# Kernel tuning notes

Measured on AMD Instinct MI355X. Metric: run time of the kernel, lower is better.

## Reference

```python
import jax, jax.numpy as jnp
import numpy as np

N = 50000      # nodes
E = 800000     # edges (avg degree 16)
IN = 128       # in_feats
HID = 32       # hidden_feats per head
H = 4          # num_heads
NEG_SLOPE = 0.2


def setup_inputs() -> dict:
    key = jax.random.key(0)
    ks = jax.random.split(key, 13)
    x = jax.random.normal(ks[0], (N, IN), jnp.float32)
    src = jax.random.randint(ks[1], (E,), 0, N, jnp.int32)
    dst = jax.random.randint(ks[2], (E,), 0, N, jnp.int32)

    def lin(k, fi, fo):
        return jax.random.normal(k, (fi, fo), jnp.float32) * (1.0 / np.sqrt(fi))

    # conv1: IN -> H*HID
    W1 = lin(ks[3], IN, H * HID)
    al1 = jax.random.normal(ks[4], (H, HID), jnp.float32) * 0.1
    ar1 = jax.random.normal(ks[5], (H, HID), jnp.float32) * 0.1
    b1 = jnp.zeros((H, HID), jnp.float32)
    # conv2: H*HID -> H*HID
    W2 = lin(ks[6], H * HID, H * HID)
    al2 = jax.random.normal(ks[7], (H, HID), jnp.float32) * 0.1
    ar2 = jax.random.normal(ks[8], (H, HID), jnp.float32) * 0.1
    b2 = jnp.zeros((H, HID), jnp.float32)
    # fc: HID -> 1
    fcW = lin(ks[9], HID, 1)
    fcb = jnp.zeros((1,), jnp.float32)
    return {"x": x, "src": src, "dst": dst,
            "W1": W1, "al1": al1, "ar1": ar1, "b1": b1,
            "W2": W2, "al2": al2, "ar2": ar2, "b2": b2,
            "fcW": fcW, "fcb": fcb}


def gat_conv(x, src, dst, W, al, ar, b):
    # x: [N, F_in] -> feat: [N, H, HID]
    feat = (x @ W).reshape(N, H, HID)
    el = jnp.sum(feat * al, axis=-1)            # [N, H]
    er = jnp.sum(feat * ar, axis=-1)            # [N, H]
    e = jax.nn.leaky_relu(el[src] + er[dst], NEG_SLOPE)  # [E, H]
    # segment softmax over incoming edges of each dst node
    m = jax.ops.segment_max(e, dst, num_segments=N)      # [N, H]
    ex = jnp.exp(e - m[dst])                              # [E, H]
    denom = jax.ops.segment_sum(ex, dst, num_segments=N)  # [N, H]
    alpha = ex / denom[dst]                                # [E, H]
    msg = feat[src] * alpha[:, :, None]                    # [E, H, HID]
    out = jax.ops.segment_sum(msg, dst, num_segments=N)   # [N, H, HID]
    return out + b[None, :, :]


def reference(x, src, dst, W1, al1, ar1, b1, W2, al2, ar2, b2, fcW, fcb):
    h = gat_conv(x, src, dst, W1, al1, ar1, b1).reshape(N, H * HID)
    h = jax.nn.relu(h)
    # dropout(0.5) is identity in eval mode
    h = gat_conv(h, src, dst, W2, al2, ar2, b2).mean(axis=1)  # [N, HID]
    return h @ fcW + fcb                                       # [N, 1]
```

## Files before the change

### kernel.cpp

```cpp
#include <hip/hip_runtime.h>
#include <hip/hip_fp16.h>

#define LEAK 0.2f
#define CAP 64
#define CS 16

static __device__ inline int swz(int c, int j) {
    int qb = j >> 3, r = j & 7;
    return c * 144 + qb * 8 + (qb >> 2) * 4 + r;
}
static __device__ inline unsigned q4(float4 v, float is) {
    int x0 = __float2int_rn(v.x * is) + 128; x0 = min(max(x0, 0), 255);
    int x1 = __float2int_rn(v.y * is) + 128; x1 = min(max(x1, 0), 255);
    int x2 = __float2int_rn(v.z * is) + 128; x2 = min(max(x2, 0), 255);
    int x3 = __float2int_rn(v.w * is) + 128; x3 = min(max(x3, 0), 255);
    return (unsigned)x0 | ((unsigned)x1 << 8) | ((unsigned)x2 << 16) | ((unsigned)x3 << 24);
}

__global__ __launch_bounds__(256) void k0(
    int* __restrict__ cnt,
    const float* __restrict__ W2, const float* __restrict__ al2,
    const float* __restrict__ ar2, const float* __restrict__ fcW,
    const float* __restrict__ b2, float* __restrict__ WfT,
    float* __restrict__ bc, int N, int zb) {
    const int b = blockIdx.x;
    const int t = threadIdx.x;
    if (b < zb) {
        int i = b * 256 + t;
        if (i < N * (CS / 4)) ((int4*)cnt)[i] = make_int4(0, 0, 0, 0);
        return;
    }
    int idx = (b - zb) * 256 + t;
    if (idx < 1536) {
        int c = idx >> 7, k = idx & 127;
        int h = c & 3, sel = c >> 2;
        const float* vec = (sel == 0) ? (al2 + 32 * h)
                         : (sel == 1) ? (ar2 + 32 * h) : fcW;
        float s = 0.f;
#pragma unroll 8
        for (int m = 0; m < 32; m++) s += W2[k * 128 + 32 * h + m] * vec[m];
        WfT[c * 128 + k] = s;
    } else if (idx < 1540) {
        int h = idx - 1536;
        float s = 0.f;
        for (int m = 0; m < 32; m++) s += b2[h * 32 + m] * fcW[m];
        bc[h] = s;
    }
}

__global__ __launch_bounds__(256) void k_ell(
    const int* __restrict__ src, const int* __restrict__ dst,
    int* __restrict__ cnt, unsigned short* __restrict__ ell,
    int E, int N, int R) {
    const int part = blockIdx.x & 7;
    const int rank = blockIdx.x >> 3;
    const int S = (N + 7) >> 3;
    const int lo = part * S;
    const int hi = (lo + S < N) ? (lo + S) : N;
    const int per = (E + R - 1) / R;
    const int e0 = rank * per;
    const int e1 = (e0 + per < E) ? (e0 + per) : E;
    int e = e0 + threadIdx.x;
    for (; e + 768 < e1; e += 1024) {
        int d0 = dst[e];       int d1 = dst[e + 256];
        int d2 = dst[e + 512]; int d3 = dst[e + 768];
        if (d0 >= lo && d0 < hi) {
            int pos = atomicAdd(&cnt[d0 * CS], 1);
            if (pos < CAP) ell[(size_t)d0 * CAP + pos] = (unsigned short)src[e];
        }
        if (d1 >= lo && d1 < hi) {
            int pos = atomicAdd(&cnt[d1 * CS], 1);
            if (pos < CAP) ell[(size_t)d1 * CAP + pos] = (unsigned short)src[e + 256];
        }
        if (d2 >= lo && d2 < hi) {
            int pos = atomicAdd(&cnt[d2 * CS], 1);
            if (pos < CAP) ell[(size_t)d2 * CAP + pos] = (unsigned short)src[e + 512];
        }
        if (d3 >= lo && d3 < hi) {
            int pos = atomicAdd(&cnt[d3 * CS], 1);
            if (pos < CAP) ell[(size_t)d3 * CAP + pos] = (unsigned short)src[e + 768];
        }
    }
    for (; e < e1; e += 256) {
        int d = dst[e];
        if (d >= lo && d < hi) {
            int pos = atomicAdd(&cnt[d * CS], 1);
            if (pos < CAP) ell[(size_t)d * CAP + pos] = (unsigned short)src[e];
        }
    }
}

__global__ __launch_bounds__(256, 4) void k1g(
    const float* __restrict__ X, const float* __restrict__ W,
    const float* __restrict__ al, const float* __restrict__ ar,
    float2* __restrict__ elsc2, float* __restrict__ er_nh,
    unsigned* __restrict__ fq8, int N) {
    __shared__ float sW[32 * 128];
    __shared__ float sXT[32 * 64];
    const int t = threadIdx.x;
    const int r0 = blockIdx.x * 64;
    const int tx = t & 15;
    const int ty = t >> 4;
    const float4* X4 = (const float4*)X;
    const float4* W4 = (const float4*)W;
    float4* sW4 = (float4*)sW;
    const float4* sXT4 = (const float4*)sXT;

    float4 acc[4][2];
#pragma unroll
    for (int r = 0; r < 4; r++) {
        acc[r][0] = make_float4(0.f, 0.f, 0.f, 0.f);
        acc[r][1] = make_float4(0.f, 0.f, 0.f, 0.f);
    }
    for (int ks = 0; ks < 4; ++ks) {
        if (ks) __syncthreads();
#pragma unroll
        for (int i = 0; i < 4; i++) {
            int idx = i * 256 + t;
            sW4[idx] = W4[1024 * ks + idx];
        }
#pragma unroll
        for (int i = 0; i < 2; i++) {
            int idx = i * 256 + t;
            int row = idx >> 3;
            int kq = idx & 7;
            float4 v = make_float4(0.f, 0.f, 0.f, 0.f);
            if (r0 + row < N) v = X4[(size_t)(r0 + row) * 32 + ks * 8 + kq];
            int sc = ((row >> 2) ^ kq) * 4 + (row & 3);
            sXT[(4 * kq + 0) * 64 + sc] = v.x;
            sXT[(4 * kq + 1) * 64 + sc] = v.y;
            sXT[(4 * kq + 2) * 64 + sc] = v.z;
            sXT[(4 * kq + 3) * 64 + sc] = v.w;
        }
        __syncthreads();
#pragma unroll 4
        for (int k = 0; k < 32; k++) {
            float4 w0 = sW4[k * 32 + tx];
            float4 w1 = sW4[k * 32 + 16 + tx];
            float4 x0 = sXT4[k * 16 + (ty ^ (k >> 2))];
            float xs[4] = {x0.x, x0.y, x0.z, x0.w};
#pragma unroll
            for (int r = 0; r < 4; r++) {
                acc[r][0].x += xs[r] * w0.x; acc[r][0].y += xs[r] * w0.y;
                acc[r][0].z += xs[r] * w0.z; acc[r][0].w += xs[r] * w0.w;
                acc[r][1].x += xs[r] * w1.x; acc[r][1].y += xs[r] * w1.y;
                acc[r][1].z += xs[r] * w1.z; acc[r][1].w += xs[r] * w1.w;
            }
        }
    }
    const float4* al4p = (const float4*)al;
    const float4* ar4p = (const float4*)ar;
    float4 alA = al4p[tx], alB = al4p[16 + tx];
    float4 arA = ar4p[tx], arB = ar4p[16 + tx];
#pragma unroll
    for (int r = 0; r < 4; r++) {
        int row = r0 + ty * 4 + r;
        bool ok = row < N;
        float4 a0 = acc[r][0], a1 = acc[r][1];
        float m = fmaxf(fmaxf(fmaxf(fabsf(a0.x), fabsf(a0.y)),
                              fmaxf(fabsf(a0.z), fabsf(a0.w))),
                        fmaxf(fmaxf(fabsf(a1.x), fabsf(a1.y)),
                              fmaxf(fabsf(a1.z), fabsf(a1.w))));
#pragma unroll
        for (int off = 1; off < 16; off <<= 1) m = fmaxf(m, __shfl_xor(m, off));
        float scale = m * (1.f / 127.f);
        float is = (m > 0.f) ? (127.f / m) : 0.f;
        if (ok) {
            fq8[(size_t)row * 32 + tx] = q4(a0, is);
            fq8[(size_t)row * 32 + 16 + tx] = q4(a1, is);
        }
        float elA = a0.x * alA.x + a0.y * alA.y + a0.z * alA.z + a0.w * alA.w;
        float erA = a0.x * arA.x + a0.y * arA.y + a0.z * arA.z + a0.w * arA.w;
        float elB = a1.x * alB.x + a1.y * alB.y + a1.z * alB.z + a1.w * alB.w;
        float erB = a1.x * arB.x + a1.y * arB.y + a1.z * arB.z + a1.w * arB.w;
#pragma unroll
        for (int off = 1; off < 8; off <<= 1) {
            elA += __shfl_xor(elA, off); erA += __shfl_xor(erA, off);
            elB += __shfl_xor(elB, off); erB += __shfl_xor(erB, off);
        }
        if (ok && tx == 0) {
            elsc2[row * 4 + 0] = make_float2(elA, scale);
            elsc2[row * 4 + 2] = make_float2(elB, scale);
            er_nh[row * 4 + 0] = erA;
            er_nh[row * 4 + 2] = erB;
        }
        if (ok && tx == 8) {
            elsc2[row * 4 + 1] = make_float2(elA, scale);
            elsc2[row * 4 + 3] = make_float2(elB, scale);
            er_nh[row * 4 + 1] = erA;
            er_nh[row * 4 + 3] = erB;
        }
    }
}

__global__ __launch_bounds__(256) void k_agg1P(
    const unsigned* __restrict__ fq8, const float2* __restrict__ elsc2,
    const float* __restrict__ er_nh, const unsigned short* __restrict__ ell,
    const int* __restrict__ cnt, const float* __restrict__ b1,
    const float* __restrict__ WfT, float2* __restrict__ Pag,
    float* __restrict__ er2, int N) {
    __shared__ float sWf[12 * 144];
    for (int i = threadIdx.x; i < 1536; i += 256)
        sWf[swz(i >> 7, i & 127)] = WfT[i];
    __syncthreads();
    const int wave = threadIdx.x >> 6, lane = threadIdx.x & 63;
    const int nsub = lane >> 4, q = lane & 15, h = q >> 2;
    const int wbase = q * 8 + (q >> 2) * 4;
    const uint2* fq2 = (const uint2*)fq8;

    const int n = blockIdx.x * 16 + wave * 4 + nsub;
    const bool nok = n < N;
    const int nc = nok ? n : (N - 1);
    int deg = nok ? cnt[n * CS] : 0; if (deg > CAP) deg = CAP;
    float er = nok ? er_nh[n * 4 + h] : 0.f;
    const unsigned short* row = ell + (size_t)nc * CAP;

    int dm = deg;
    dm = max(dm, __shfl_xor(dm, 16));
    dm = max(dm, __shfl_xor(dm, 32));

    float acc[8] = {0.f, 0.f, 0.f, 0.f, 0.f, 0.f, 0.f, 0.f};
    float den = 0.f, wss = 0.f;
    for (int jt = 0; jt < dm; jt += 16) {
        int s_all = (jt + q < CAP) ? (int)row[jt + q] : 0;
        int lim = dm - jt; if (lim > 16) lim = 16;
        for (int u = 0; u < lim; u += 8) {
            int sv[8]; float2 esv[8]; uint2 fv[8];
#pragma unroll
            for (int v = 0; v < 8; v++) {
                int jj = jt + u + v;
                int s = __shfl(s_all, (lane & 48) | ((u + v) & 15));
                sv[v] = (jj < deg) ? s : 0;
            }
#pragma unroll
            for (int v = 0; v < 8; v++) esv[v] = elsc2[sv[v] * 4 + h];
#pragma unroll
            for (int v = 0; v < 8; v++) fv[v] = fq2[(size_t)sv[v] * 16 + q];
#pragma unroll
            for (int v = 0; v < 8; v++) {
                int jj = jt + u + v;
                bool valid = jj < deg;
                float e = esv[v].x + er;
                e = fmaxf(e, LEAK * e);
                float w = valid ? __expf(e) : 0.f;
                float ws = w * esv[v].y;
                unsigned ua = fv[v].x, ub = fv[v].y;
                acc[0] += ws * (float)(ua & 0xff);
                acc[1] += ws * (float)((ua >> 8) & 0xff);
                acc[2] += ws * (float)((ua >> 16) & 0xff);
                acc[3] += ws * (float)(ua >> 24);
                acc[4] += ws * (float)(ub & 0xff);
                acc[5] += ws * (float)((ub >> 8) & 0xff);
                acc[6] += ws * (float)((ub >> 16) & 0xff);
                acc[7] += ws * (float)(ub >> 24);
                den += w; wss += ws;
            }
        }
    }
    float inv = (den > 0.f) ? (1.f / den) : 0.f;
    float off128 = 128.f * wss;
    float4 b1a = ((const float4*)b1)[q * 2];
    float4 b1b = ((const float4*)b1)[q * 2 + 1];
    float hv[8];
    hv[0] = fmaxf((acc[0] - off128) * inv + b1a.x, 0.f);
    hv[1] = fmaxf((acc[1] - off128) * inv + b1a.y, 0.f);
    hv[2] = fmaxf((acc[2] - off128) * inv + b1a.z, 0.f);
    hv[3] = fmaxf((acc[3] - off128) * inv + b1a.w, 0.f);
    hv[4] = fmaxf((acc[4] - off128) * inv + b1b.x, 0.f);
    hv[5] = fmaxf((acc[5] - off128) * inv + b1b.y, 0.f);
    hv[6] = fmaxf((acc[6] - off128) * inv + b1b.z, 0.f);
    hv[7] = fmaxf((acc[7] - off128) * inv + b1b.w, 0.f);
    float p[12];
#pragma unroll
    for (int c = 0; c < 12; c++) {
        const float* wr = sWf + c * 144 + wbase;
        float4 wa = *(const float4*)wr;
        float4 wb = *(const float4*)(wr + 4);
        p[c] = hv[0] * wa.x + hv[1] * wa.y + hv[2] * wa.z + hv[3] * wa.w
             + hv[4] * wb.x + hv[5] * wb.y + hv[6] * wb.z + hv[7] * wb.w;
    }
#pragma unroll
    for (int off = 1; off < 16; off <<= 1) {
#pragma unroll
        for (int c = 0; c < 12; c++) p[c] += __shfl_xor(p[c], off);
    }
    if (nok) {
        if (q < 4) Pag[(size_t)n * 4 + q] = make_float2(p[q], p[8 + q]);
        else if (q < 8) er2[(size_t)n * 4 + (q - 4)] = p[q];
    }
}

__global__ __launch_bounds__(256) void k_agg2(
    const float2* __restrict__ Pag, const float* __restrict__ er2,
    const unsigned short* __restrict__ ell, const int* __restrict__ cnt,
    const float* __restrict__ bc, const float* __restrict__ fcb,
    float* __restrict__ out, int N) {
    int idx = blockIdx.x * 256 + threadIdx.x;
    int n = idx >> 2, h = idx & 3;
    if (n >= N) return;
    int deg = cnt[n * CS]; if (deg > CAP) deg = CAP;
    float er = er2[(size_t)n * 4 + h];
    const unsigned short* row = ell + (size_t)n * CAP;
    float num = 0.f, den = 0.f;
    int j = 0, d8 = deg & ~7;
    for (; j < d8; j += 8) {
        ushort4 sa = *(const ushort4*)(row + j);
        ushort4 sb = *(const ushort4*)(row + j + 4);
        int sv[8] = {sa.x, sa.y, sa.z, sa.w, sb.x, sb.y, sb.z, sb.w};
        float2 g[8];
#pragma unroll
        for (int v = 0; v < 8; v++) g[v] = Pag[(size_t)sv[v] * 4 + h];
#pragma unroll
        for (int v = 0; v < 8; v++) {
            float e = g[v].x + er; e = fmaxf(e, LEAK * e);
            float w = __expf(e);
            num += w * g[v].y; den += w;
        }
    }
    for (; j < deg; ++j) {
        int s = row[j];
        float2 gg = Pag[(size_t)s * 4 + h];
        float e = gg.x + er; e = fmaxf(e, LEAK * e);
        float w = __expf(e);
        num += w * gg.y; den += w;
    }
    float r = (den > 0.f) ? (num / den) : 0.f;
    r += bc[h];
    r += __shfl_xor(r, 1);
    r += __shfl_xor(r, 2);
    if (h == 0) out[n] = 0.25f * r + fcb[0];
}

extern "C" void kernel_launch(void* const* d_in, const int* in_sizes, int n_in,
                              void* d_out, int out_size, void* d_ws, size_t ws_size,
                              hipStream_t stream) {
    const float* x   = (const float*)d_in[0];
    const int* src   = (const int*)d_in[1];
    const int* dst   = (const int*)d_in[2];
    const float* W1  = (const float*)d_in[3];
    const float* al1 = (const float*)d_in[4];
    const float* ar1 = (const float*)d_in[5];
    const float* b1  = (const float*)d_in[6];
    const float* W2  = (const float*)d_in[7];
    const float* al2 = (const float*)d_in[8];
    const float* ar2 = (const float*)d_in[9];
    const float* b2  = (const float*)d_in[10];
    const float* fcW = (const float*)d_in[11];
    const float* fcb = (const float*)d_in[12];
    float* out = (float*)d_out;

    const int N = in_sizes[0] / 128;
    const int E = in_sizes[1];

    char* w = (char*)d_ws;
    size_t off = 0;
    auto alloc = [&](size_t bytes) {
        void* p = w + off;
        off = (off + bytes + 255) & ~(size_t)255;
        return p;
    };
    unsigned* fq8  = (unsigned*)alloc((size_t)N * 32 * 4);
    float2* elsc2  = (float2*)alloc((size_t)N * 4 * 8);
    float* er_nh   = (float*)alloc((size_t)N * 4 * 4);
    float2* Pag    = (float2*)alloc((size_t)N * 4 * 8);
    float* er2     = (float*)alloc((size_t)N * 4 * 4);
    float* WfT     = (float*)alloc((size_t)(12 * 128 + 4) * 4);
    float* bc      = WfT + 12 * 128;
    int* cnt       = (int*)alloc((size_t)N * CS * 4);
    unsigned short* ell = (unsigned short*)alloc((size_t)N * CAP * 2);

    const int zb = (N * (CS / 4) + 255) / 256;
    const int gtiles = (N + 63) / 64;
    const int R = 256;

    k0<<<zb + 7, 256, 0, stream>>>(
        cnt, W2, al2, ar2, fcW, b2, WfT, bc, N, zb);
    k_ell<<<8 * R, 256, 0, stream>>>(src, dst, cnt, ell, E, N, R);
    k1g<<<gtiles, 256, 0, stream>>>(
        x, W1, al1, ar1, elsc2, er_nh, fq8, N);
    k_agg1P<<<(N + 15) / 16, 256, 0, stream>>>(
        fq8, elsc2, er_nh, ell, cnt, b1, WfT, Pag, er2, N);
    k_agg2<<<(N * 4 + 255) / 256, 256, 0, stream>>>(
        Pag, er2, ell, cnt, bc, fcb, out, N);
}
```

Baseline: 200.0 us.

## Fuse ELL build and first-layer GEMM into one interleaved launch

```diff
diff --git a/kernel.cpp b/kernel.cpp
--- a/kernel.cpp
+++ b/kernel.cpp
@@ -48,57 +48,65 @@
     }
 }
 
-__global__ __launch_bounds__(256) void k_ell(
-    const int* __restrict__ src, const int* __restrict__ dst,
-    int* __restrict__ cnt, unsigned short* __restrict__ ell,
-    int E, int N, int R) {
-    const int part = blockIdx.x & 7;
-    const int rank = blockIdx.x >> 3;
-    const int S = (N + 7) >> 3;
-    const int lo = part * S;
-    const int hi = (lo + S < N) ? (lo + S) : N;
-    const int per = (E + R - 1) / R;
-    const int e0 = rank * per;
-    const int e1 = (e0 + per < E) ? (e0 + per) : E;
-    int e = e0 + threadIdx.x;
-    for (; e + 768 < e1; e += 1024) {
-        int d0 = dst[e];       int d1 = dst[e + 256];
-        int d2 = dst[e + 512]; int d3 = dst[e + 768];
-        if (d0 >= lo && d0 < hi) {
-            int pos = atomicAdd(&cnt[d0 * CS], 1);
-            if (pos < CAP) ell[(size_t)d0 * CAP + pos] = (unsigned short)src[e];
-        }
-        if (d1 >= lo && d1 < hi) {
-            int pos = atomicAdd(&cnt[d1 * CS], 1);
-            if (pos < CAP) ell[(size_t)d1 * CAP + pos] = (unsigned short)src[e + 256];
-        }
-        if (d2 >= lo && d2 < hi) {
-            int pos = atomicAdd(&cnt[d2 * CS], 1);
-            if (pos < CAP) ell[(size_t)d2 * CAP + pos] = (unsigned short)src[e + 512];
-        }
-        if (d3 >= lo && d3 < hi) {
-            int pos = atomicAdd(&cnt[d3 * CS], 1);
-            if (pos < CAP) ell[(size_t)d3 * CAP + pos] = (unsigned short)src[e + 768];
-        }
-    }
-    for (; e < e1; e += 256) {
-        int d = dst[e];
-        if (d >= lo && d < hi) {
-            int pos = atomicAdd(&cnt[d * CS], 1);
-            if (pos < CAP) ell[(size_t)d * CAP + pos] = (unsigned short)src[e];
-        }
-    }
-}
-
-__global__ __launch_bounds__(256, 4) void k1g(
+__global__ __launch_bounds__(256, 4) void k_eg(
     const float* __restrict__ X, const float* __restrict__ W,
     const float* __restrict__ al, const float* __restrict__ ar,
     float2* __restrict__ elsc2, float* __restrict__ er_nh,
-    unsigned* __restrict__ fq8, int N) {
+    unsigned* __restrict__ fq8,
+    const int* __restrict__ src, const int* __restrict__ dst,
+    int* __restrict__ cnt, unsigned short* __restrict__ ell,
+    int N, int E, int R, int GO, int T) {
     __shared__ float sW[32 * 128];
     __shared__ float sXT[32 * 64];
+    const int b = blockIdx.x;
     const int t = threadIdx.x;
-    const int r0 = blockIdx.x * 64;
+    const int o = b >> 3;
+    const int g0 = (o * GO) / T;
+    const bool isGemm = ((o + 1) * GO) / T > g0;
+
+    if (!isGemm) {
+        const int part = b & 7;
+        const int rank = o - g0;
+        const int S = (N + 7) >> 3;
+        const int lo = part * S;
+        const int hi = (lo + S < N) ? (lo + S) : N;
+        const int per = (E + R - 1) / R;
+        const int e0 = rank * per;
+        const int e1 = (e0 + per < E) ? (e0 + per) : E;
+        int e = e0 + t;
+        for (; e + 768 < e1; e += 1024) {
+            int d0 = dst[e];       int d1 = dst[e + 256];
+            int d2 = dst[e + 512]; int d3 = dst[e + 768];
+            if (d0 >= lo && d0 < hi) {
+                int pos = atomicAdd(&cnt[d0 * CS], 1);
+                if (pos < CAP) ell[(size_t)d0 * CAP + pos] = (unsigned short)src[e];
+            }
+            if (d1 >= lo && d1 < hi) {
+                int pos = atomicAdd(&cnt[d1 * CS], 1);
+                if (pos < CAP) ell[(size_t)d1 * CAP + pos] = (unsigned short)src[e + 256];
+            }
+            if (d2 >= lo && d2 < hi) {
+                int pos = atomicAdd(&cnt[d2 * CS], 1);
+                if (pos < CAP) ell[(size_t)d2 * CAP + pos] = (unsigned short)src[e + 512];
+            }
+            if (d3 >= lo && d3 < hi) {
+                int pos = atomicAdd(&cnt[d3 * CS], 1);
+                if (pos < CAP) ell[(size_t)d3 * CAP + pos] = (unsigned short)src[e + 768];
+            }
+        }
+        for (; e < e1; e += 256) {
+            int d = dst[e];
+            if (d >= lo && d < hi) {
+                int pos = atomicAdd(&cnt[d * CS], 1);
+                if (pos < CAP) ell[(size_t)d * CAP + pos] = (unsigned short)src[e];
+            }
+        }
+        return;
+    }
+
+    const int tile = g0 * 8 + (b & 7);
+    const int r0 = tile * 64;
+    if (r0 >= N) return;
     const int tx = t & 15;
     const int ty = t >> 4;
     const float4* X4 = (const float4*)X;
@@ -372,12 +380,14 @@
     const int zb = (N * (CS / 4) + 255) / 256;
     const int gtiles = (N + 63) / 64;
     const int R = 256;
+    const int GO = (gtiles + 7) / 8;
+    const int T = R + GO;
 
     k0<<<zb + 7, 256, 0, stream>>>(
         cnt, W2, al2, ar2, fcW, b2, WfT, bc, N, zb);
-    k_ell<<<8 * R, 256, 0, stream>>>(src, dst, cnt, ell, E, N, R);
-    k1g<<<gtiles, 256, 0, stream>>>(
-        x, W1, al1, ar1, elsc2, er_nh, fq8, N);
+    k_eg<<<8 * T, 256, 0, stream>>>(
+        x, W1, al1, ar1, elsc2, er_nh, fq8,
+        src, dst, cnt, ell, N, E, R, GO, T);
     k_agg1P<<<(N + 15) / 16, 256, 0, stream>>>(
         fq8, elsc2, er_nh, ell, cnt, b1, WfT, Pag, er2, N);
     k_agg2<<<(N * 4 + 255) / 256, 256, 0, stream>>>(
```

Measured after the change: 188.6 us. 5.7% less time.
